# Performance work log

Measured on AMD Instinct MI355X. Metric: run time of the kernel, lower is better.

Reference implementation:

```python
import jax, jax.numpy as jnp
import numpy as np


def setup_inputs() -> dict:
    key = jax.random.key(0)
    ks = jax.random.split(key, 10)
    B, S, D = 16, 2048, 256
    return {
        "x": jax.random.normal(ks[0], (B, S, D), dtype=jnp.float32),
        "noise": jax.random.normal(ks[1], (B, S, D), dtype=jnp.float32),
        "alpha1": jax.random.normal(ks[2], (D,), dtype=jnp.float32),
        "alpha2": jax.random.normal(ks[3], (D,), dtype=jnp.float32),
        "W_ttt": jax.random.normal(ks[4], (D, D), dtype=jnp.float32),
        "W_proj": jax.random.normal(ks[5], (D, D), dtype=jnp.float32),
        "ff_alpha": jax.random.normal(ks[6], (D,), dtype=jnp.float32),
        "ff_beta": jax.random.normal(ks[7], (D,), dtype=jnp.float32),
        "ff_gamma": jax.random.normal(ks[8], (1,), dtype=jnp.float32),
        "ff_eta": jax.random.normal(ks[9], (1,), dtype=jnp.float32),
    }


def _ttt(W, m, noise):
    # m, noise: [B, S, D]; sequential SGD on W over the sequence axis.
    B, S, D = m.shape
    scale = 2.0 / (B * D)  # d(mse)/d(pred) factor

    def step(W, inp):
        state, eps = inp                      # [B, D] each
        train = state + eps
        diff = train @ W.T - state            # pred - label, [B, D]
        grad = scale * (diff.T @ train)       # dL/dW, [D, D]
        Wn = W - 0.01 * grad
        return Wn, state @ Wn.T               # readout with updated W

    _, outs = jax.lax.scan(step, W, (jnp.swapaxes(m, 0, 1), jnp.swapaxes(noise, 0, 1)))
    return jnp.swapaxes(outs, 0, 1)           # [B, S, D]


def reference(x, noise, alpha1, alpha2, W_ttt, W_proj, ff_alpha, ff_beta, ff_gamma, ff_eta):
    # memory path: VecDyT norm then TTT (readouts are detached in torch)
    m = jnp.tanh(alpha1 * x)
    mem = jax.lax.stop_gradient(_ttt(W_ttt, m, noise))

    # feedforward path: VecDyT norm then FFUnit
    v = jnp.tanh(alpha2 * x)
    u = ff_gamma * jax.nn.gelu(ff_alpha * v, approximate=False) + ff_eta * jnp.sin(ff_beta * v)
    g = u * (v @ W_proj.T)

    return mem + g
```

## Files before the change

### kernel.cpp

```cpp
#include <hip/hip_runtime.h>

typedef unsigned short u16;
typedef unsigned int u32;
typedef __attribute__((ext_vector_type(8))) short bf16x8;
typedef __attribute__((ext_vector_type(4))) float f32x4;

#define SB 16
#define SS 2048
#define SD 256
#define CC 16
#define NCH (SS / CC)
#define KAPPA 4.8828125e-6f
#define RP 24
#define SLOT 65536

__device__ __forceinline__ u16 f2bf(float f) {
  u32 u = __float_as_uint(f);
  u = (u + 0x7FFFu + ((u >> 16) & 1u)) >> 16;
  return (u16)u;
}
__device__ __forceinline__ float bf2f(u16 u) { return __uint_as_float((u32)u << 16); }

__device__ __forceinline__ bf16x8 ldfrag(const u16* p) {
  union { uint4 u; bf16x8 f; } cv;
  cv.u = *(const uint4*)p;
  return cv.f;
}
__device__ __forceinline__ bf16x8 asfrag(uint4 q) {
  union { uint4 u; bf16x8 f; } cv;
  cv.u = q;
  return cv.f;
}
__device__ __forceinline__ f32x4 mfma16(bf16x8 a, bf16x8 b, f32x4 c) {
  return __builtin_amdgcn_mfma_f32_16x16x32_bf16(a, b, c, 0, 0, 0);
}

__global__ __launch_bounds__(256) void prep_kernel(
    const float* __restrict__ x, const float* __restrict__ noise,
    const float* __restrict__ a1, const float* __restrict__ a2,
    u16* __restrict__ train, u16* __restrict__ state, u16* __restrict__ trainT,
    u16* __restrict__ vh, u16* __restrict__ vl) {
  size_t i4 = (size_t)blockIdx.x * 256 + threadIdx.x;
  size_t base = i4 * 4;
  int d = (int)(base & 255);
  int t = (int)((base >> 8) & 2047);
  int b = (int)(base >> 19);
  float4 xv = *(const float4*)(x + base);
  float4 nv = *(const float4*)(noise + base);
  float4 av = *(const float4*)(a1 + d);
  float4 a2v = *(const float4*)(a2 + d);
  float m0 = tanhf(av.x * xv.x);
  float m1 = tanhf(av.y * xv.y);
  float m2 = tanhf(av.z * xv.z);
  float m3 = tanhf(av.w * xv.w);
  size_t dst = ((size_t)t * SB + b) * SD + d;
  ushort4 tr, st;
  tr.x = f2bf(m0 + nv.x); tr.y = f2bf(m1 + nv.y);
  tr.z = f2bf(m2 + nv.z); tr.w = f2bf(m3 + nv.w);
  st.x = f2bf(m0); st.y = f2bf(m1); st.z = f2bf(m2); st.w = f2bf(m3);
  *(ushort4*)(train + dst) = tr;
  *(ushort4*)(state + dst) = st;
  size_t tb = ((size_t)t * SD + d) * SB + b;
  trainT[tb + 0 * SB] = tr.x;
  trainT[tb + 1 * SB] = tr.y;
  trainT[tb + 2 * SB] = tr.z;
  trainT[tb + 3 * SB] = tr.w;
  float v0 = tanhf(a2v.x * xv.x);
  float v1 = tanhf(a2v.y * xv.y);
  float v2 = tanhf(a2v.z * xv.z);
  float v3 = tanhf(a2v.w * xv.w);
  ushort4 h, l;
  h.x = f2bf(v0); l.x = f2bf(v0 - bf2f(h.x));
  h.y = f2bf(v1); l.y = f2bf(v1 - bf2f(h.y));
  h.z = f2bf(v2); l.z = f2bf(v2 - bf2f(h.z));
  h.w = f2bf(v3); l.w = f2bf(v3 - bf2f(h.w));
  *(ushort4*)(vh + base) = h;
  *(ushort4*)(vl + base) = l;
}

__global__ __launch_bounds__(256) void wsplit_kernel(
    const float* __restrict__ Wp, u16* __restrict__ Wph, u16* __restrict__ Wpl) {
  size_t i = ((size_t)blockIdx.x * 256 + threadIdx.x) * 4;
  float4 v = *(const float4*)(Wp + i);
  ushort4 h, l;
  h.x = f2bf(v.x); l.x = f2bf(v.x - bf2f(h.x));
  h.y = f2bf(v.y); l.y = f2bf(v.y - bf2f(h.y));
  h.z = f2bf(v.z); l.z = f2bf(v.z - bf2f(h.z));
  h.w = f2bf(v.w); l.w = f2bf(v.w - bf2f(h.w));
  *(ushort4*)(Wph + i) = h;
  *(ushort4*)(Wpl + i) = l;
}

__global__ __launch_bounds__(256) void gram2ff_kernel(
    const u16* __restrict__ tr, const u16* __restrict__ st,
    u16* __restrict__ AG, u16* __restrict__ LbG,
    const u16* __restrict__ vh, const u16* __restrict__ vl,
    const u16* __restrict__ Wph, const u16* __restrict__ Wpl,
    const float* __restrict__ ffa, const float* __restrict__ ffb,
    const float* __restrict__ ffg_, const float* __restrict__ ffe_,
    float* __restrict__ out) {
  const int tid = threadIdx.x;

  if (blockIdx.x < 2048) {
    const int cb = blockIdx.x;
    const int c = cb >> 4, t = cb & 15;
    const int lane = tid & 63, wv = tid >> 6;
    const int lr = lane & 15, lq = lane >> 4;
    const size_t Tt = (size_t)cb;
    bf16x8 trF[8], stF[8];
#pragma unroll
    for (int k = 0; k < 8; ++k) {
      trF[k] = ldfrag(tr + (Tt * 16 + lr) * 256 + k * 32 + lq * 8);
      stF[k] = ldfrag(st + (Tt * 16 + lr) * 256 + k * 32 + lq * 8);
    }
    for (int ii = 0; ii < 2; ++ii) {
      const int sp = wv + ii * 4;
      u16* dA = AG + ((size_t)cb * 8 + sp) * 512;
      u16* dL = LbG + ((size_t)cb * 8 + sp) * 512;
#pragma unroll
      for (int h = 0; h < 2; ++h) {
        const int s = 2 * sp + h;
        f32x4 accA = {0.f, 0.f, 0.f, 0.f}, accL = {0.f, 0.f, 0.f, 0.f};
        if (s <= t) {
          const u16* bsrc = tr + ((size_t)(c * 16 + s) * 16 + lr) * 256 + lq * 8;
#pragma unroll
          for (int k = 0; k < 8; ++k) {
            bf16x8 bk = ldfrag(bsrc + k * 32);
            if (s < t) accA = mfma16(trF[k], bk, accA);
            accL = mfma16(stF[k], bk, accL);
          }
        }
#pragma unroll
        for (int r = 0; r < 4; ++r) {
          int idx = (lq * 4 + r) * 32 + h * 16 + lr;
          dA[idx] = (s < t) ? f2bf(accA[r]) : (u16)0;
          dL[idx] = (s <= t) ? f2bf(accL[r]) : (u16)0;
        }
      }
    }
    return;
  }

  const int fb = blockIdx.x - 2048;
  const int gm0 = ((fb & 7) + 8 * (fb >> 5)) * 64;
  const int gn0 = ((fb >> 3) & 3) * 64;
  const int lane = tid & 63, w = tid >> 6;
  const int lr = lane & 15, lq = lane >> 4;

  bf16x8 ah[8], al[8];
  {
    const u16* vhp = vh + (size_t)(gm0 + w * 16 + lr) * 256 + lq * 8;
    const u16* vlp = vl + (size_t)(gm0 + w * 16 + lr) * 256 + lq * 8;
#pragma unroll
    for (int kb = 0; kb < 8; ++kb) {
      ah[kb] = ldfrag(vhp + kb * 32);
      al[kb] = ldfrag(vlp + kb * 32);
    }
  }
  const float ga = ffg_[0], et = ffe_[0];
#pragma unroll
  for (int cb = 0; cb < 4; ++cb) {
    const u16* bhp = Wph + (size_t)(gn0 + cb * 16 + lr) * 256 + lq * 8;
    const u16* blp = Wpl + (size_t)(gn0 + cb * 16 + lr) * 256 + lq * 8;
    f32x4 acc = {0.f, 0.f, 0.f, 0.f};
#pragma unroll
    for (int kb = 0; kb < 8; ++kb) {
      bf16x8 bh = ldfrag(bhp + kb * 32);
      bf16x8 bl = ldfrag(blp + kb * 32);
      acc = mfma16(ah[kb], bh, acc);
      acc = mfma16(al[kb], bh, acc);
      acc = mfma16(ah[kb], bl, acc);
    }
#pragma unroll
    for (int r = 0; r < 4; ++r) {
      const int row = gm0 + w * 16 + lq * 4 + r;
      const int col = gn0 + cb * 16 + lr;
      const size_t vi = (size_t)row * 256 + col;
      float v = bf2f(vh[vi]) + bf2f(vl[vi]);
      float z = ffa[col] * v;
      float gelu = 0.5f * z * (1.0f + erff(z * 0.70710678118654752f));
      float u = ga * gelu + et * sinf(ffb[col] * v);
      out[vi] = u * acc[r];
    }
  }
}

__global__ __launch_bounds__(512) void phaseA_kernel(
    const u16* __restrict__ tr, const u16* __restrict__ st,
    const u16* __restrict__ trT, const u16* __restrict__ AG,
    u16* __restrict__ Dt, u16* __restrict__ Db, u16* __restrict__ Qb) {
  __shared__ u16 StT[CC][16 * RP];
  __shared__ u16 YtL[CC][16 * RP];
  __shared__ u16 ZtL[CC][16 * RP];
  const int tid = threadIdx.x;
  const int lane = tid & 63;
  const int w = tid >> 6;
  const int id = blockIdx.x;
  const int c = (id & 7) + 8 * (id >> 7);
  const int d1b = (id >> 3) & 15;
  const int lr = lane & 15;
  const int lq = lane >> 4;

  uint4 agR[2][8];
#pragma unroll
  for (int u = 0; u < 2; ++u) {
    const u16* ag = AG + ((size_t)(c * 16 + w + 8 * u) * 8) * 512 + lr * 32 + lq * 8;
#pragma unroll
    for (int sp = 0; sp < 8; ++sp) agR[u][sp] = *(const uint4*)(ag + sp * 512);
  }
  u16 sraw[2][4];
  float xs[2][4];
#pragma unroll
  for (int u = 0; u < 2; ++u) {
    const size_t T = (size_t)c * CC + w + 8 * u;
    ushort4 pk;
#pragma unroll
    for (int r = 0; r < 4; ++r) {
      size_t idx = (T * 16 + lq * 4 + r) * 256 + d1b * 16 + lr;
      sraw[u][r] = st[idx];
      xs[u][r] = bf2f(tr[idx]);
      ((u16*)&pk)[r] = sraw[u][r];
    }
    *(ushort4*)(&StT[w + 8 * u][lr * RP + lq * 4]) = pk;
  }
  __syncthreads();

#pragma unroll
  for (int u = 0; u < 2; ++u) {
    f32x4 a1 = {0.f, 0.f, 0.f, 0.f}, a2 = {0.f, 0.f, 0.f, 0.f};
#pragma unroll
    for (int sp = 0; sp < 8; ++sp) {
      const int s0 = 2 * sp + (lq >> 1);
      bf16x8 xb = ldfrag(trT + ((size_t)(c * CC + s0) * 256 + d1b * 16 + lr) * 16 +
                         (lq & 1) * 8);
      bf16x8 sb = ldfrag(&StT[s0][lr * RP + (lq & 1) * 8]);
      a1 = mfma16(asfrag(agR[u][sp]), xb, a1);
      a2 = mfma16(asfrag(agR[u][sp]), sb, a2);
    }
    ushort4 py, pz;
#pragma unroll
    for (int r = 0; r < 4; ++r) {
      ((u16*)&py)[r] = f2bf(xs[u][r] - KAPPA * a1[r]);
      ((u16*)&pz)[r] = f2bf(bf2f(sraw[u][r]) - KAPPA * a2[r]);
    }
    *(ushort4*)(&YtL[w + 8 * u][lr * RP + lq * 4]) = py;
    *(ushort4*)(&ZtL[w + 8 * u][lr * RP + lq * 4]) = pz;
  }
  __syncthreads();

  bf16x8 yf[8], zf[8];
#pragma unroll
  for (int sp = 0; sp < 8; ++sp) {
    yf[sp] = ldfrag(&YtL[2 * sp + (lq >> 1)][lr * RP + (lq & 1) * 8]);
    zf[sp] = ldfrag(&ZtL[2 * sp + (lq >> 1)][lr * RP + (lq & 1) * 8]);
  }
  const size_t base = (size_t)c * SLOT;
#pragma unroll
  for (int u = 0; u < 2; ++u) {
    const int d2b = w + 8 * u;
    f32x4 da = {0.f, 0.f, 0.f, 0.f}, qa = {0.f, 0.f, 0.f, 0.f};
#pragma unroll
    for (int sp = 0; sp < 8; ++sp) {
      bf16x8 xb = ldfrag(trT + ((size_t)(c * CC + 2 * sp + (lq >> 1)) * 256 +
                                d2b * 16 + lr) * 16 + (lq & 1) * 8);
      da = mfma16(yf[sp], xb, da);
      qa = mfma16(zf[sp], xb, qa);
    }
    ushort4 dpk;
#pragma unroll
    for (int r = 0; r < 4; ++r) {
      const u16 dv = f2bf(-KAPPA * da[r]);
      ((u16*)&dpk)[r] = dv;
      Db[base + (size_t)(d1b * 16 + lq * 4 + r) * 256 + d2b * 16 + lr] = dv;
      Qb[base + (size_t)(d1b * 16 + lq * 4 + r) * 256 + d2b * 16 + lr] =
          f2bf(KAPPA * qa[r]);
    }
    *(ushort4*)(Dt + base + (size_t)(d2b * 16 + lr) * 256 + d1b * 16 + lq * 4) = dpk;
  }
}

__global__ __launch_bounds__(512) void kq_kernel(
    const u16* __restrict__ Dt, u16* __restrict__ Qb, int lev) {
  const int id = blockIdx.x;
  const int qn = (id & 7) + 8 * (id >> 7);
  const int rb = (id >> 3) & 15;
  const int half = 1 << (lev - 1);
  const int blk = qn >> (lev - 1), win = qn & (half - 1);
  const int i = blk * half * 2 + half + win;
  const int j = blk * half * 2 + half - 1;
  u16* Qi = Qb + (size_t)i * SLOT;
  const u16* Qj = Qb + (size_t)j * SLOT;
  const u16* Dti = Dt + (size_t)i * SLOT;
  const int lane = threadIdx.x & 63, w = threadIdx.x >> 6;
  const int lr = lane & 15, lq = lane >> 4;
  bf16x8 aq[8];
#pragma unroll
  for (int kb = 0; kb < 8; ++kb)
    aq[kb] = ldfrag(Qj + (size_t)(rb * 16 + lr) * 256 + kb * 32 + lq * 8);
#pragma unroll
  for (int u = 0; u < 2; ++u) {
    const int cb = w + 8 * u;
    f32x4 acc = {0.f, 0.f, 0.f, 0.f};
#pragma unroll
    for (int kb = 0; kb < 8; ++kb) {
      bf16x8 bf = ldfrag(Dti + (size_t)(cb * 16 + lr) * 256 + kb * 32 + lq * 8);
      acc = mfma16(aq[kb], bf, acc);
    }
#pragma unroll
    for (int r = 0; r < 4; ++r) {
      size_t idx = (size_t)(rb * 16 + lq * 4 + r) * 256 + cb * 16 + lr;
      float v = acc[r] + bf2f(Qj[idx]) + bf2f(Qi[idx]);
      Qi[idx] = f2bf(v);
    }
  }
}

__global__ __launch_bounds__(512) void kdt_kernel(
    u16* __restrict__ Dt, u16* __restrict__ Db, int lev) {
  const int id = blockIdx.x;
  const int qn = (id & 7) + 8 * (id >> 7);
  const int rb = (id >> 3) & 15;
  const int half = 1 << (lev - 1);
  const int blk = qn >> (lev - 1), win = qn & (half - 1);
  const int i = blk * half * 2 + half + win;
  const int j = blk * half * 2 + half - 1;
  u16* Dti = Dt + (size_t)i * SLOT;
  const u16* Dtj = Dt + (size_t)j * SLOT;
  u16* Dbi = Db + (size_t)i * SLOT;
  const u16* Dbj = Db + (size_t)j * SLOT;
  const int lane = threadIdx.x & 63, w = threadIdx.x >> 6;
  const int lr = lane & 15, lq = lane >> 4;
  bf16x8 ad[8];
#pragma unroll
  for (int kb = 0; kb < 8; ++kb)
    ad[kb] = ldfrag(Dti + (size_t)(rb * 16 + lr) * 256 + kb * 32 + lq * 8);
  float oldv[2][4];
#pragma unroll
  for (int u = 0; u < 2; ++u) {
    const int cb = w + 8 * u;
#pragma unroll
    for (int r = 0; r < 4; ++r) {
      size_t idx = (size_t)(rb * 16 + lq * 4 + r) * 256 + cb * 16 + lr;
      oldv[u][r] = bf2f(Dtj[idx]) + bf2f(Dti[idx]);
    }
  }
  __syncthreads();
#pragma unroll
  for (int u = 0; u < 2; ++u) {
    const int cb = w + 8 * u;
    f32x4 acc = {0.f, 0.f, 0.f, 0.f};
#pragma unroll
    for (int kb = 0; kb < 8; ++kb) {
      bf16x8 bf = ldfrag(Dbj + (size_t)(cb * 16 + lr) * 256 + kb * 32 + lq * 8);
      acc = mfma16(ad[kb], bf, acc);
    }
    ushort4 mir;
#pragma unroll
    for (int r = 0; r < 4; ++r) {
      const u16 nv = f2bf(acc[r] + oldv[u][r]);
      ((u16*)&mir)[r] = nv;
      Dti[(size_t)(rb * 16 + lq * 4 + r) * 256 + cb * 16 + lr] = nv;
    }
    *(ushort4*)(Dbi + (size_t)(cb * 16 + lr) * 256 + rb * 16 + lq * 4) = mir;
  }
}

__global__ __launch_bounds__(512) void wstart_kernel(
    const float* __restrict__ Wttt, const u16* __restrict__ Dt,
    const u16* __restrict__ Qb, u16* __restrict__ Wsb) {
  const int c = blockIdx.x;
  const int tid = threadIdx.x;
  const int lane = tid & 63, w = tid >> 6;
  const int lr = lane & 15, lq = lane >> 4;
  if (c == 0) {
    for (int i = tid; i < SLOT / 4; i += 512) {
      float4 v = *(const float4*)(Wttt + (size_t)i * 4);
      ushort4 o;
      o.x = f2bf(v.x); o.y = f2bf(v.y); o.z = f2bf(v.z); o.w = f2bf(v.w);
      *(ushort4*)(Wsb + (size_t)i * 4) = o;
    }
    return;
  }
  const size_t ex = (size_t)(c - 1) * SLOT;
  u16* Wc = Wsb + (size_t)c * SLOT;
#pragma unroll
  for (int ui = 0; ui < 2; ++ui) {
    const int rb = w + 8 * ui;
    bf16x8 wf[8];
#pragma unroll
    for (int kb = 0; kb < 8; ++kb) {
      const float* wp = Wttt + (size_t)(rb * 16 + lr) * 256 + kb * 32 + lq * 8;
      float4 w0 = *(const float4*)(wp);
      float4 w1 = *(const float4*)(wp + 4);
      union { u16 s[8]; bf16x8 f; } cv;
      cv.s[0] = f2bf(w0.x); cv.s[1] = f2bf(w0.y);
      cv.s[2] = f2bf(w0.z); cv.s[3] = f2bf(w0.w);
      cv.s[4] = f2bf(w1.x); cv.s[5] = f2bf(w1.y);
      cv.s[6] = f2bf(w1.z); cv.s[7] = f2bf(w1.w);
      wf[kb] = cv.f;
    }
    for (int cb = 0; cb < 16; ++cb) {
      f32x4 acc = {0.f, 0.f, 0.f, 0.f};
#pragma unroll
      for (int kb = 0; kb < 8; ++kb) {
        bf16x8 bf = ldfrag(Dt + ex + (size_t)(cb * 16 + lr) * 256 + kb * 32 + lq * 8);
        acc = mfma16(wf[kb], bf, acc);
      }
#pragma unroll
      for (int r = 0; r < 4; ++r) {
        size_t idx = (size_t)(rb * 16 + lq * 4 + r) * 256 + cb * 16 + lr;
        float v = Wttt[idx] + acc[r] + bf2f(Qb[ex + idx]);
        Wc[idx] = f2bf(v);
      }
    }
  }
}

__global__ __launch_bounds__(512) void phaseC_kernel(
    const u16* __restrict__ tr, const u16* __restrict__ st,
    const u16* __restrict__ AG, const u16* __restrict__ LbG,
    const u16* __restrict__ Wsb, float* __restrict__ out) {
  __shared__ u16 RpL[CC][16 * RP];
  __shared__ u16 DpL[CC][16 * RP];
  __shared__ u16 WbL[16][268];

  const int tid = threadIdx.x;
  const int lane = tid & 63;
  const int w = tid >> 6;
  const int id = blockIdx.x;
  const int c = (id & 7) + 8 * (id >> 7);
  const int d1b = (id >> 3) & 15;
  const int lr = lane & 15;
  const int lq = lane >> 4;

  {
    const int row = tid >> 5, col = (tid & 31) * 8;
    *(uint4*)&WbL[row][col] =
        *(const uint4*)(Wsb + (size_t)c * SLOT + (size_t)(d1b * 16 + row) * 256 + col);
  }
  __syncthreads();

  uint4 agR[2][8];
#pragma unroll
  for (int u = 0; u < 2; ++u) {
    const u16* ag = AG + ((size_t)(c * 16 + w + 8 * u) * 8) * 512 + lr * 32 + lq * 8;
#pragma unroll
    for (int sp = 0; sp < 8; ++sp) agR[u][sp] = *(const uint4*)(ag + sp * 512);
  }
  uint4 trR[2][8], stR[2][8];
  float sub[2][4];
#pragma unroll
  for (int u = 0; u < 2; ++u) {
    const size_t T = (size_t)c * CC + w + 8 * u;
    const u16* trt = tr + (T * 16 + lr) * 256 + lq * 8;
    const u16* stt = st + (T * 16 + lr) * 256 + lq * 8;
#pragma unroll
    for (int k = 0; k < 8; ++k) {
      trR[u][k] = *(const uint4*)(trt + k * 32);
      stR[u][k] = *(const uint4*)(stt + k * 32);
    }
#pragma unroll
    for (int r = 0; r < 4; ++r)
      sub[u][r] = bf2f(st[(T * 16 + lq * 4 + r) * 256 + d1b * 16 + lr]);
  }

  f32x4 rhsF[2], qF[2];
#pragma unroll
  for (int u = 0; u < 2; ++u) {
    f32x4 racc = {0.f, 0.f, 0.f, 0.f}, qacc = {0.f, 0.f, 0.f, 0.f};
#pragma unroll
    for (int k = 0; k < 8; ++k) {
      bf16x8 wb = ldfrag(&WbL[lr][k * 32 + lq * 8]);
      racc = mfma16(asfrag(trR[u][k]), wb, racc);
      qacc = mfma16(asfrag(stR[u][k]), wb, qacc);
    }
#pragma unroll
    for (int r = 0; r < 4; ++r) racc[r] -= sub[u][r];
    rhsF[u] = racc; qF[u] = qacc;
    ushort4 pk;
    pk.x = f2bf(racc.x); pk.y = f2bf(racc.y);
    pk.z = f2bf(racc.z); pk.w = f2bf(racc.w);
    *(ushort4*)(&RpL[w + 8 * u][lr * RP + lq * 4]) = pk;
  }
  __syncthreads();

  uint4 lbR[2][8];
#pragma unroll
  for (int u = 0; u < 2; ++u) {
    const u16* lb = LbG + ((size_t)(c * 16 + w + 8 * u) * 8) * 512 + lr * 32 + lq * 8;
#pragma unroll
    for (int sp = 0; sp < 8; ++sp) lbR[u][sp] = *(const uint4*)(lb + sp * 512);
  }

#pragma unroll
  for (int u = 0; u < 2; ++u) {
    f32x4 acc = {0.f, 0.f, 0.f, 0.f};
#pragma unroll
    for (int sp = 0; sp < 8; ++sp) {
      bf16x8 bf = ldfrag(&RpL[2 * sp + (lq >> 1)][lr * RP + (lq & 1) * 8]);
      acc = mfma16(asfrag(agR[u][sp]), bf, acc);
    }
    ushort4 pk;
#pragma unroll
    for (int r = 0; r < 4; ++r) {
      float dv = rhsF[u][r] - KAPPA * acc[r];
      ((u16*)&pk)[r] = f2bf(-KAPPA * dv);
    }
    *(ushort4*)(&DpL[w + 8 * u][lr * RP + lq * 4]) = pk;
  }
  __syncthreads();

  float gp[2][4];
#pragma unroll
  for (int u = 0; u < 2; ++u) {
    const size_t T = (size_t)c * CC + w + 8 * u;
#pragma unroll
    for (int r = 0; r < 4; ++r)
      gp[u][r] = out[((size_t)(lq * 4 + r) * SS + T) * SD + d1b * 16 + lr];
  }
#pragma unroll
  for (int u = 0; u < 2; ++u) {
    const size_t T = (size_t)c * CC + w + 8 * u;
    f32x4 acc = qF[u];
#pragma unroll
    for (int sp = 0; sp < 8; ++sp) {
      bf16x8 bf = ldfrag(&DpL[2 * sp + (lq >> 1)][lr * RP + (lq & 1) * 8]);
      acc = mfma16(asfrag(lbR[u][sp]), bf, acc);
    }
#pragma unroll
    for (int r = 0; r < 4; ++r) {
      size_t oi = ((size_t)(lq * 4 + r) * SS + T) * SD + d1b * 16 + lr;
      out[oi] = acc[r] + gp[u][r];
    }
  }
}

extern "C" void kernel_launch(void* const* d_in, const int* in_sizes, int n_in,
                              void* d_out, int out_size, void* d_ws, size_t ws_size,
                              hipStream_t stream) {
  const float* x     = (const float*)d_in[0];
  const float* noise = (const float*)d_in[1];
  const float* a1    = (const float*)d_in[2];
  const float* a2    = (const float*)d_in[3];
  const float* Wttt  = (const float*)d_in[4];
  const float* Wproj = (const float*)d_in[5];
  const float* ffa   = (const float*)d_in[6];
  const float* ffb   = (const float*)d_in[7];
  const float* ffg   = (const float*)d_in[8];
  const float* ffe   = (const float*)d_in[9];
  float* out = (float*)d_out;

  const size_t N = (size_t)SB * SS * SD;
  u16* tr  = (u16*)d_ws;
  u16* st  = tr + N;
  u16* trT = st + N;
  u16* AG  = trT + N;
  u16* LbG = AG + N;
  u16* Dt  = LbG + N;
  u16* Qb  = Dt + N;
  u16* Db  = Qb + N;
  u16* Wsb = trT;
  u16* vhB = Dt;
  u16* vlB = Qb;
  u16* Wph = Db;
  u16* Wpl = Db + SLOT;

  prep_kernel<<<8192, 256, 0, stream>>>(x, noise, a1, a2, tr, st, trT, vhB, vlB);
  wsplit_kernel<<<64, 256, 0, stream>>>(Wproj, Wph, Wpl);
  gram2ff_kernel<<<4096, 256, 0, stream>>>(tr, st, AG, LbG, vhB, vlB, Wph, Wpl,
                                           ffa, ffb, ffg, ffe, out);
  phaseA_kernel<<<2048, 512, 0, stream>>>(tr, st, trT, AG, Dt, Db, Qb);
  for (int lev = 1; lev <= 7; ++lev) {
    kq_kernel<<<1024, 512, 0, stream>>>(Dt, Qb, lev);
    kdt_kernel<<<1024, 512, 0, stream>>>(Dt, Db, lev);
  }
  wstart_kernel<<<128, 512, 0, stream>>>(Wttt, Dt, Qb, Wsb);
  phaseC_kernel<<<2048, 512, 0, stream>>>(tr, st, AG, LbG, Wsb, out);
}
```

Baseline: 894.4 us.

## Fuse per-level kq and kdt kernels into one LDS-staged kernel per level

```diff
diff --git a/kernel.cpp b/kernel.cpp
--- a/kernel.cpp
+++ b/kernel.cpp
@@ -102,8 +102,10 @@
   const int tid = threadIdx.x;
 
   if (blockIdx.x < 2048) {
-    const int cb = blockIdx.x;
-    const int c = cb >> 4, t = cb & 15;
+    const int id = blockIdx.x;
+    const int c = (id & 7) + 8 * (id >> 7);
+    const int t = (id >> 3) & 15;
+    const int cb = c * 16 + t;
     const int lane = tid & 63, wv = tid >> 6;
     const int lr = lane & 15, lq = lane >> 4;
     const size_t Tt = (size_t)cb;
@@ -279,47 +281,10 @@
   }
 }
 
-__global__ __launch_bounds__(512) void kq_kernel(
-    const u16* __restrict__ Dt, u16* __restrict__ Qb, int lev) {
-  const int id = blockIdx.x;
-  const int qn = (id & 7) + 8 * (id >> 7);
-  const int rb = (id >> 3) & 15;
-  const int half = 1 << (lev - 1);
-  const int blk = qn >> (lev - 1), win = qn & (half - 1);
-  const int i = blk * half * 2 + half + win;
-  const int j = blk * half * 2 + half - 1;
-  u16* Qi = Qb + (size_t)i * SLOT;
-  const u16* Qj = Qb + (size_t)j * SLOT;
-  const u16* Dti = Dt + (size_t)i * SLOT;
-  const int lane = threadIdx.x & 63, w = threadIdx.x >> 6;
-  const int lr = lane & 15, lq = lane >> 4;
-  bf16x8 aq[8];
-#pragma unroll
-  for (int kb = 0; kb < 8; ++kb)
-    aq[kb] = ldfrag(Qj + (size_t)(rb * 16 + lr) * 256 + kb * 32 + lq * 8);
-#pragma unroll
-  for (int u = 0; u < 2; ++u) {
-    const int cb = w + 8 * u;
-    f32x4 acc = {0.f, 0.f, 0.f, 0.f};
-#pragma unroll
-    for (int kb = 0; kb < 8; ++kb) {
-      bf16x8 bf = ldfrag(Dti + (size_t)(cb * 16 + lr) * 256 + kb * 32 + lq * 8);
-      acc = mfma16(aq[kb], bf, acc);
-    }
-#pragma unroll
-    for (int r = 0; r < 4; ++r) {
-      size_t idx = (size_t)(rb * 16 + lq * 4 + r) * 256 + cb * 16 + lr;
-      float v = acc[r] + bf2f(Qj[idx]) + bf2f(Qi[idx]);
-      Qi[idx] = f2bf(v);
-    }
-  }
-}
-
-__global__ __launch_bounds__(512) void kdt_kernel(
-    u16* __restrict__ Dt, u16* __restrict__ Db, int lev) {
-  const int id = blockIdx.x;
-  const int qn = (id & 7) + 8 * (id >> 7);
-  const int rb = (id >> 3) & 15;
+__global__ __launch_bounds__(512) void klev_kernel(
+    u16* __restrict__ Dt, u16* __restrict__ Db, u16* __restrict__ Qb, int lev) {
+  __shared__ u16 S[65536];
+  const int qn = blockIdx.x;
   const int half = 1 << (lev - 1);
   const int blk = qn >> (lev - 1), win = qn & (half - 1);
   const int i = blk * half * 2 + half + win;
@@ -328,40 +293,89 @@
   const u16* Dtj = Dt + (size_t)j * SLOT;
   u16* Dbi = Db + (size_t)i * SLOT;
   const u16* Dbj = Db + (size_t)j * SLOT;
-  const int lane = threadIdx.x & 63, w = threadIdx.x >> 6;
+  u16* Qi = Qb + (size_t)i * SLOT;
+  const u16* Qj = Qb + (size_t)j * SLOT;
+  const int tid = threadIdx.x;
+  const int lane = tid & 63, w = tid >> 6;
   const int lr = lane & 15, lq = lane >> 4;
-  bf16x8 ad[8];
-#pragma unroll
-  for (int kb = 0; kb < 8; ++kb)
-    ad[kb] = ldfrag(Dti + (size_t)(rb * 16 + lr) * 256 + kb * 32 + lq * 8);
-  float oldv[2][4];
-#pragma unroll
-  for (int u = 0; u < 2; ++u) {
-    const int cb = w + 8 * u;
-#pragma unroll
-    for (int r = 0; r < 4; ++r) {
-      size_t idx = (size_t)(rb * 16 + lq * 4 + r) * 256 + cb * 16 + lr;
-      oldv[u][r] = bf2f(Dtj[idx]) + bf2f(Dti[idx]);
-    }
-  }
-  __syncthreads();
-#pragma unroll
-  for (int u = 0; u < 2; ++u) {
-    const int cb = w + 8 * u;
-    f32x4 acc = {0.f, 0.f, 0.f, 0.f};
+
+  for (int it = tid; it < 8192; it += 512) {
+    int row = it >> 5, c16 = it & 31;
+    uint4 v = *(const uint4*)(Dti + (size_t)row * 256 + c16 * 8);
+    int off = row * 512 + ((c16 * 16) ^ ((row & 7) << 4));
+    *(uint4*)((char*)S + off) = v;
+  }
+  __syncthreads();
+
+#pragma unroll
+  for (int ui = 0; ui < 2; ++ui) {
+    const int rb = w + 8 * ui;
+    bf16x8 aq[8];
+#pragma unroll
+    for (int kb = 0; kb < 8; ++kb)
+      aq[kb] = ldfrag(Qj + (size_t)(rb * 16 + lr) * 256 + kb * 32 + lq * 8);
+    for (int cb = 0; cb < 16; ++cb) {
+      f32x4 acc = {0.f, 0.f, 0.f, 0.f};
+#pragma unroll
+      for (int kb = 0; kb < 8; ++kb) {
+        const int row = cb * 16 + lr;
+        const int colb = kb * 64 + lq * 16;
+        bf16x8 bf = *(const bf16x8*)((const char*)S + row * 512 +
+                                     (colb ^ ((row & 7) << 4)));
+        acc = mfma16(aq[kb], bf, acc);
+      }
+#pragma unroll
+      for (int r = 0; r < 4; ++r) {
+        size_t idx = (size_t)(rb * 16 + lq * 4 + r) * 256 + cb * 16 + lr;
+        Qi[idx] = f2bf(acc[r] + bf2f(Qj[idx]) + bf2f(Qi[idx]));
+      }
+    }
+  }
+  bf16x8 ad[2][8];
+#pragma unroll
+  for (int ui = 0; ui < 2; ++ui) {
+    const int rb = w + 8 * ui;
 #pragma unroll
     for (int kb = 0; kb < 8; ++kb) {
-      bf16x8 bf = ldfrag(Dbj + (size_t)(cb * 16 + lr) * 256 + kb * 32 + lq * 8);
-      acc = mfma16(ad[kb], bf, acc);
-    }
-    ushort4 mir;
-#pragma unroll
-    for (int r = 0; r < 4; ++r) {
-      const u16 nv = f2bf(acc[r] + oldv[u][r]);
-      ((u16*)&mir)[r] = nv;
-      Dti[(size_t)(rb * 16 + lq * 4 + r) * 256 + cb * 16 + lr] = nv;
-    }
-    *(ushort4*)(Dbi + (size_t)(cb * 16 + lr) * 256 + rb * 16 + lq * 4) = mir;
+      const int row = rb * 16 + lr;
+      const int colb = kb * 64 + lq * 16;
+      ad[ui][kb] = *(const bf16x8*)((const char*)S + row * 512 +
+                                    (colb ^ ((row & 7) << 4)));
+    }
+  }
+  __syncthreads();
+
+  for (int it = tid; it < 8192; it += 512) {
+    int row = it >> 5, c16 = it & 31;
+    uint4 v = *(const uint4*)(Dbj + (size_t)row * 256 + c16 * 8);
+    int off = row * 512 + ((c16 * 16) ^ ((row & 7) << 4));
+    *(uint4*)((char*)S + off) = v;
+  }
+  __syncthreads();
+
+#pragma unroll
+  for (int ui = 0; ui < 2; ++ui) {
+    const int rb = w + 8 * ui;
+    for (int cb = 0; cb < 16; ++cb) {
+      f32x4 acc = {0.f, 0.f, 0.f, 0.f};
+#pragma unroll
+      for (int kb = 0; kb < 8; ++kb) {
+        const int row = cb * 16 + lr;
+        const int colb = kb * 64 + lq * 16;
+        bf16x8 bf = *(const bf16x8*)((const char*)S + row * 512 +
+                                     (colb ^ ((row & 7) << 4)));
+        acc = mfma16(ad[ui][kb], bf, acc);
+      }
+      ushort4 mir;
+#pragma unroll
+      for (int r = 0; r < 4; ++r) {
+        size_t idx = (size_t)(rb * 16 + lq * 4 + r) * 256 + cb * 16 + lr;
+        const u16 nv = f2bf(acc[r] + bf2f(Dtj[idx]) + bf2f(Dti[idx]));
+        ((u16*)&mir)[r] = nv;
+        Dti[idx] = nv;
+      }
+      *(ushort4*)(Dbi + (size_t)(cb * 16 + lr) * 256 + rb * 16 + lq * 4) = mir;
+    }
   }
 }
 
@@ -570,10 +584,8 @@
   gram2ff_kernel<<<4096, 256, 0, stream>>>(tr, st, AG, LbG, vhB, vlB, Wph, Wpl,
                                            ffa, ffb, ffg, ffe, out);
   phaseA_kernel<<<2048, 512, 0, stream>>>(tr, st, trT, AG, Dt, Db, Qb);
-  for (int lev = 1; lev <= 7; ++lev) {
-    kq_kernel<<<1024, 512, 0, stream>>>(Dt, Qb, lev);
-    kdt_kernel<<<1024, 512, 0, stream>>>(Dt, Db, lev);
-  }
+  for (int lev = 1; lev <= 7; ++lev)
+    klev_kernel<<<64, 512, 0, stream>>>(Dt, Db, Qb, lev);
   wstart_kernel<<<128, 512, 0, stream>>>(Wttt, Dt, Qb, Wsb);
   phaseC_kernel<<<2048, 512, 0, stream>>>(tr, st, AG, LbG, Wsb, out);
 }
```

Result: slower. 1.004 ms (+12.2%).
